# Kernel optimization log

Hardware: AMD Instinct MI355X
Metric: run time of the kernel (lower is better)

## Reference

```python
import jax, jax.numpy as jnp
import numpy as np

N_NUM = 8
N_CAT = 4
CARD = 100
D_NUM = 16
D_CAT = 16
D_OUT = N_NUM * D_NUM + N_CAT * D_CAT  # 192
D_HID = 256
TEMP = 1.0


def setup_inputs() -> dict:
    key = jax.random.key(0)
    ks = jax.random.split(key, 12)
    B, N = 512, 131072
    x_num = jax.random.normal(ks[0], (B, N_NUM), dtype=jnp.float32)
    x_cat = jax.random.randint(ks[1], (B, N_CAT), 0, CARD)
    cand_x_num = jax.random.normal(ks[2], (N, N_NUM), dtype=jnp.float32)
    cand_x_cat = jax.random.randint(ks[3], (N, N_CAT), 0, CARD)
    cand_y = jax.random.uniform(ks[4], (N, 10), dtype=jnp.float32)
    s = 0.05
    W_num = jax.random.normal(ks[5], (N_NUM, D_NUM), dtype=jnp.float32) * s
    b_num = jax.random.normal(ks[6], (N_NUM, D_NUM), dtype=jnp.float32) * s
    emb = jax.random.normal(ks[7], (N_CAT, CARD, D_CAT), dtype=jnp.float32) * s
    W1 = jax.random.normal(ks[8], (D_OUT, D_HID), dtype=jnp.float32) * s
    b1 = jnp.zeros((D_HID,), dtype=jnp.float32)
    W2 = jax.random.normal(ks[9], (D_HID, D_OUT), dtype=jnp.float32) * s
    b2 = jnp.zeros((D_OUT,), dtype=jnp.float32)
    return dict(x_num=x_num, x_cat=x_cat, cand_x_num=cand_x_num,
                cand_x_cat=cand_x_cat, cand_y=cand_y, W_num=W_num, b_num=b_num,
                emb=emb, W1=W1, b1=b1, W2=W2, b2=b2)


def _encode(x_num, x_cat, W_num, b_num, emb):
    # per-numerical-feature linear embedding: [B, n_num, d_num]
    num_e = x_num[:, :, None] * W_num[None] + b_num[None]
    # categorical lookup: emb[f, x_cat[:, f]] -> [B, n_cat, d_cat]
    cat_e = emb[jnp.arange(N_CAT)[None, :], x_cat]
    B = x_num.shape[0]
    return jnp.concatenate([num_e.reshape(B, -1), cat_e.reshape(B, -1)], axis=-1)


def _block(z, W1, b1, W2, b2):
    # residual MLP block: d_out -> hidden -> d_out
    return z + jax.nn.relu(z @ W1 + b1) @ W2 + b2


def reference(x_num, x_cat, cand_x_num, cand_x_cat, cand_y,
              W_num, b_num, emb, W1, b1, W2, b2):
    x = _encode(x_num, x_cat, W_num, b_num, emb)            # [B, d]
    c = _encode(cand_x_num, cand_x_cat, W_num, b_num, emb)  # [N, d]
    x = _block(x, W1, b1, W2, b2)
    c = _block(c, W1, b1, W2, b2)
    d2 = (jnp.sum(x * x, axis=-1)[:, None] + jnp.sum(c * c, axis=-1)[None, :]
          - 2.0 * (x @ c.T))
    dist = jnp.sqrt(jnp.maximum(d2, 0.0)) / TEMP            # [B, N]
    probs = jax.nn.softmax(-dist, axis=-1)
    return probs @ cand_y                                    # [B, 10]
```

## Files before the change

### kernel.cpp

```cpp
#include <hip/hip_runtime.h>
#include <hip/hip_bf16.h>

typedef __bf16 bf16;
typedef __attribute__((ext_vector_type(8))) __bf16 bf16x8;
typedef __attribute__((ext_vector_type(4))) __bf16 bf16x4;
typedef __attribute__((ext_vector_type(4))) float f32x4;

#define NQ     512
#define NC     131072
#define DIM    192
#define HID    256
#define NY     10
#define NSLICE 512

#define KL2E   2.0813689810056077f
#define N2KL2E -4.1627379620112154f

#define OFF_W1B 0u
#define OFF_W2B (OFF_W1B + 98304u)
#define OFF_XE8 (OFF_W2B + 98304u)
#define OFF_X2  (OFF_XE8 + 98304u)
#define OFF_CE8 (OFF_X2 + 2048u)
#define OFF_C2  (OFF_CE8 + 25165824u)
#define OFF_P   (OFF_C2 + 524288u)
#define OFF_YB  (OFF_P + 12582912u)

__global__ __launch_bounds__(256) void k_prep(const float* __restrict__ W1,
                                              const float* __restrict__ W2,
                                              const float* __restrict__ cy,
                                              bf16* __restrict__ W1B,
                                              bf16* __restrict__ W2B,
                                              bf16* __restrict__ YB) {
  if (blockIdx.x < 384) {
    int idx = blockIdx.x * 256 + threadIdx.x;
    if (idx < 192 * 256) {
      int k = idx / 256, n = idx % 256;
      int p = (k >> 5) * 4 + ((k >> 3) & 3);
      W1B[((size_t)(p * 256 + n)) * 8 + (k & 7)] = (bf16)W1[idx];
    } else {
      int i2 = idx - 192 * 256;
      int k = i2 / 192, n = i2 % 192;
      int p = (k >> 5) * 4 + ((k >> 3) & 3);
      W2B[((size_t)(p * 192 + n)) * 8 + (k & 7)] = (bf16)W2[i2];
    }
  } else {
    int u = (blockIdx.x - 384) * 256 + threadIdx.x;
    int p32 = u >> 6, lane6 = u & 63;
    int qq = lane6 >> 4, l15 = lane6 & 15;
    bf16x8 v;
#pragma unroll
    for (int jj = 0; jj < 8; jj++) {
      int cand = p32 * 32 + qq * 8 + jj;
      float x = (l15 < 10) ? cy[(size_t)cand * NY + l15] : (l15 == 10 ? 1.f : 0.f);
      v[jj] = (bf16)x;
    }
    *(bf16x8*)&YB[(size_t)u * 8] = v;
  }
}

__global__ __launch_bounds__(256, 3) void k_encode(
    const float* __restrict__ xnq, const int* __restrict__ xcq,
    const float* __restrict__ xnc, const int* __restrict__ xcc,
    const float* __restrict__ Wn, const float* __restrict__ bn,
    const float* __restrict__ emb, const float* __restrict__ b1,
    const float* __restrict__ b2, const bf16* __restrict__ W1B,
    const bf16* __restrict__ W2B, unsigned char* __restrict__ ce8,
    unsigned char* __restrict__ xe8, float* __restrict__ x2v,
    float* __restrict__ c2v) {
  __shared__ alignas(16) bf16 zt[64][200];
  __shared__ alignas(16) bf16 hth[64][136];
  __shared__ float n2l[64];
  unsigned char* zs = (unsigned char*)&hth[0][0];

  const int t = threadIdx.x;
  const bool isq = blockIdx.x < 8;
  const int row0 = (isq ? blockIdx.x : blockIdx.x - 8) * 64;
  const float* __restrict__ xn = isq ? xnq : xnc;
  const int* __restrict__ xc = isq ? xcq : xcc;
  const int lane = t & 63, w = t >> 6;
  const int l15 = lane & 15, q = lane >> 4;

  if (t < 64) n2l[t] = 0.f;

  {
    const int g = row0 + lane;
    float2 xv2 = *(const float2*)&xn[(size_t)g * 8 + 2 * w];
    int cv = xc[g * 4 + w];
#pragma unroll
    for (int f01 = 0; f01 < 2; f01++) {
      int f = 2 * w + f01;
      float xv = f01 ? xv2.y : xv2.x;
      f32x4 wv[4], bv[4];
#pragma unroll
      for (int i = 0; i < 4; i++) {
        wv[i] = *(const f32x4*)&Wn[f * 16 + i * 4];
        bv[i] = *(const f32x4*)&bn[f * 16 + i * 4];
      }
      bf16x8 p0, p1;
#pragma unroll
      for (int u = 0; u < 8; u++) {
        p0[u] = (bf16)(xv * wv[u >> 2][u & 3] + bv[u >> 2][u & 3]);
        p1[u] = (bf16)(xv * wv[2 + (u >> 2)][u & 3] + bv[2 + (u >> 2)][u & 3]);
      }
      *(bf16x8*)&zt[lane][f * 16] = p0;
      *(bf16x8*)&zt[lane][f * 16 + 8] = p1;
    }
    const float* er = &emb[(size_t)(w * 100 + cv) * 16];
    f32x4 e0 = *(const f32x4*)&er[0];
    f32x4 e1 = *(const f32x4*)&er[4];
    f32x4 e2 = *(const f32x4*)&er[8];
    f32x4 e3 = *(const f32x4*)&er[12];
    bf16x8 pc0, pc1;
#pragma unroll
    for (int u = 0; u < 4; u++) {
      pc0[u] = (bf16)e0[u]; pc0[4 + u] = (bf16)e1[u];
      pc1[u] = (bf16)e2[u]; pc1[4 + u] = (bf16)e3[u];
    }
    *(bf16x8*)&zt[lane][128 + w * 16] = pc0;
    *(bf16x8*)&zt[lane][128 + w * 16 + 8] = pc1;
  }
  __syncthreads();

  f32x4 z4 = {0.f, 0.f, 0.f, 0.f};
  f32x4 acc2[4][3];
#pragma unroll
  for (int mi = 0; mi < 4; mi++)
#pragma unroll
    for (int ni = 0; ni < 3; ni++) acc2[mi][ni] = z4;

#pragma unroll
  for (int h = 0; h < 2; ++h) {
    if (h) __syncthreads();

    {
      f32x4 acc1[4][2];
#pragma unroll
      for (int mi = 0; mi < 4; mi++)
#pragma unroll
        for (int ni = 0; ni < 2; ni++) acc1[mi][ni] = z4;
#pragma unroll 2
      for (int kk = 0; kk < 192; kk += 32) {
        bf16x8 a[4], b[2];
#pragma unroll
        for (int mi = 0; mi < 4; mi++)
          a[mi] = *(const bf16x8*)&zt[mi * 16 + l15][kk + q * 8];
        const bf16* wp = &W1B[(size_t)(((kk >> 5) * 4 + q) * 256 + h * 128 + w * 32 + l15) * 8];
#pragma unroll
        for (int ni = 0; ni < 2; ni++)
          b[ni] = *(const bf16x8*)&wp[ni * 128];
#pragma unroll
        for (int mi = 0; mi < 4; mi++)
#pragma unroll
          for (int ni = 0; ni < 2; ni++)
            acc1[mi][ni] = __builtin_amdgcn_mfma_f32_16x16x32_bf16(a[mi], b[ni], acc1[mi][ni], 0, 0, 0);
      }
#pragma unroll
      for (int ni = 0; ni < 2; ni++) {
        int nl = w * 32 + ni * 16 + l15;
        float bb = b1[h * 128 + nl];
#pragma unroll
        for (int mi = 0; mi < 4; mi++)
#pragma unroll
          for (int r = 0; r < 4; r++) {
            float hv = acc1[mi][ni][r] + bb;
            hth[mi * 16 + q * 4 + r][nl] = (bf16)(hv > 0.f ? hv : 0.f);
          }
      }
    }
    __syncthreads();

#pragma unroll 2
    for (int kk2 = 0; kk2 < 128; kk2 += 32) {
      bf16x8 a[4], b[3];
#pragma unroll
      for (int mi = 0; mi < 4; mi++)
        a[mi] = *(const bf16x8*)&hth[mi * 16 + l15][kk2 + q * 8];
      const bf16* wp = &W2B[(size_t)(((h * 4 + (kk2 >> 5)) * 4 + q) * 192 + w * 48 + l15) * 8];
#pragma unroll
      for (int ni = 0; ni < 3; ni++)
        b[ni] = *(const bf16x8*)&wp[ni * 128];
#pragma unroll
      for (int mi = 0; mi < 4; mi++)
#pragma unroll
        for (int ni = 0; ni < 3; ni++)
          acc2[mi][ni] = __builtin_amdgcn_mfma_f32_16x16x32_bf16(a[mi], b[ni], acc2[mi][ni], 0, 0, 0);
    }
  }
  __syncthreads();

  {
    float nrm[4][4];
#pragma unroll
    for (int mi = 0; mi < 4; mi++)
#pragma unroll
      for (int r = 0; r < 4; r++) nrm[mi][r] = 0.f;
#pragma unroll
    for (int ni = 0; ni < 3; ni++) {
      int n = w * 48 + ni * 16 + l15;
      float bb = b2[n];
#pragma unroll
      for (int mi = 0; mi < 4; mi++)
#pragma unroll
        for (int r = 0; r < 4; r++) {
          int rr = mi * 16 + q * 4 + r;
          float v = (float)zt[rr][n] + acc2[mi][ni][r] + bb;
          int pk = __builtin_amdgcn_cvt_pk_fp8_f32(v, v, 0, false);
          zs[rr * 208 + n] = (unsigned char)(pk & 0xff);
          float vr = __builtin_amdgcn_cvt_f32_fp8(pk, 0);
          nrm[mi][r] += vr * vr;
        }
    }
#pragma unroll
    for (int mi = 0; mi < 4; mi++)
#pragma unroll
      for (int r = 0; r < 4; r++) {
        float s = nrm[mi][r];
        s += __shfl_xor(s, 1);
        s += __shfl_xor(s, 2);
        s += __shfl_xor(s, 4);
        s += __shfl_xor(s, 8);
        if (l15 == 0) atomicAdd(&n2l[mi * 16 + q * 4 + r], s);
      }
  }
  __syncthreads();

  if (isq) {
    for (int cc = w; cc < 24; cc += 4) {
      long v = *(const long*)&zs[lane * 208 + cc * 8];
      *(long*)&xe8[((size_t)cc * NQ + row0 + lane) * 8] = v;
    }
    if (t < 64) x2v[row0 + t] = n2l[t] * KL2E;
  } else {
    unsigned int* dst = (unsigned int*)(ce8 + (size_t)row0 * DIM);
#pragma unroll
    for (int i = 0; i < 12; i++) {
      int j = t + 256 * i;
      int r = j / 48, cb = (j - r * 48) * 4;
      dst[j] = *(const unsigned int*)&zs[r * 208 + cb];
    }
    if (t < 64) c2v[row0 + t] = n2l[t] * KL2E;
  }
}

__global__ __launch_bounds__(256, 3) void k_dist(
    const unsigned char* __restrict__ xe8, const float* __restrict__ x2v,
    const unsigned char* __restrict__ ce8, const float* __restrict__ c2v,
    const bf16* __restrict__ YB, float* __restrict__ P) {
  __shared__ alignas(16) unsigned char ct8[64][208];
  __shared__ alignas(16) bf16 ET[4][16][72];

  const int t = threadIdx.x;
  const int slice = blockIdx.x & (NSLICE - 1);
  const int half = blockIdx.x >> 9;
  const int n0 = slice * 256;
  const int qh = half * 256;
  const int lane = t & 63, w = t >> 6;
  const int l15 = lane & 15, q = lane >> 4;
  const int qbase = qh + w * 64;

  f32x4 z4 = {0.f, 0.f, 0.f, 0.f};
  f32x4 oacc[4];
#pragma unroll
  for (int nq = 0; nq < 4; nq++) oacc[nq] = z4;

  float x2a[4];
#pragma unroll
  for (int nq = 0; nq < 4; nq++) x2a[nq] = x2v[qbase + nq * 16 + l15];

#pragma unroll 1
  for (int c = 0; c < 4; ++c) {
    if (c) __syncthreads();
    {
      int sr = t >> 2, squ = t & 3;
      const uint4* src = (const uint4*)(ce8 + (size_t)(n0 + c * 64 + sr) * DIM + squ * 48);
      uint4* dst = (uint4*)&ct8[sr][squ * 48];
#pragma unroll
      for (int i = 0; i < 3; i++) dst[i] = src[i];
    }
    __syncthreads();

    bf16x8 yf[2];
#pragma unroll
    for (int kb = 0; kb < 2; kb++)
      yf[kb] = *(const bf16x8*)&YB[((size_t)((slice * 8) + c * 2 + kb) * 64 + lane) * 8];
    f32x4 c2r[4];
#pragma unroll
    for (int mc = 0; mc < 4; mc++)
      c2r[mc] = *(const f32x4*)&c2v[n0 + c * 64 + mc * 16 + q * 4];

    f32x4 acc[4][4];
#pragma unroll
    for (int mc = 0; mc < 4; mc++)
#pragma unroll
      for (int nq = 0; nq < 4; nq++) acc[mc][nq] = z4;

#pragma unroll 1
    for (int kk = 0; kk < 192; kk += 32) {
      long a[4], b[4];
#pragma unroll
      for (int mc = 0; mc < 4; mc++)
        a[mc] = *(const long*)&ct8[mc * 16 + l15][kk + q * 8];
      const unsigned char* xp = &xe8[(size_t)(((kk >> 5) * 4 + q) * NQ + qbase + l15) * 8];
#pragma unroll
      for (int nq = 0; nq < 4; nq++)
        b[nq] = *(const long*)&xp[nq * 128];
#pragma unroll
      for (int mc = 0; mc < 4; mc++)
#pragma unroll
        for (int nq = 0; nq < 4; nq++)
          acc[mc][nq] = __builtin_amdgcn_mfma_f32_16x16x32_fp8_fp8(a[mc], b[nq], acc[mc][nq], 0, 0, 0);
    }

#pragma unroll
    for (int nq = 0; nq < 4; ++nq) {
#pragma unroll
      for (int mc = 0; mc < 4; mc++) {
        bf16x4 ev;
#pragma unroll
        for (int r = 0; r < 4; r++) {
          float d2 = __builtin_fmaf(N2KL2E, acc[mc][nq][r], x2a[nq] + c2r[mc][r]);
          ev[r] = (bf16)__builtin_amdgcn_exp2f(-__builtin_amdgcn_sqrtf(__builtin_fabsf(d2)));
        }
        *(bf16x4*)&ET[w][l15][mc * 16 + q * 4] = ev;
      }
#pragma unroll
      for (int kb = 0; kb < 2; kb++) {
        bf16x8 a = *(const bf16x8*)&ET[w][l15][kb * 32 + q * 8];
        oacc[nq] = __builtin_amdgcn_mfma_f32_16x16x32_bf16(a, yf[kb], oacc[nq], 0, 0, 0);
      }
    }
  }

  __syncthreads();
  float* Pst = (float*)&ct8[0][0];
  if (l15 < 11) {
#pragma unroll
    for (int nq = 0; nq < 4; nq++)
#pragma unroll
      for (int r = 0; r < 4; r++) {
        int lq = w * 64 + nq * 16 + q * 4 + r;
        Pst[lq * 12 + l15] = oacc[nq][r];
      }
  }
  __syncthreads();
  {
    f32x4* Pg = (f32x4*)(P + (size_t)blockIdx.x * 3072);
    const f32x4* Ps = (const f32x4*)Pst;
#pragma unroll
    for (int i = t; i < 768; i += 256) Pg[i] = Ps[i];
  }
}

__global__ __launch_bounds__(512) void k_comb(const float* __restrict__ P,
                                              float* __restrict__ out) {
  __shared__ float red[8][11];
  const int t = threadIdx.x;
  const int qy = blockIdx.x;
  const int lane = t & 63, w = t >> 6;

  const float* p = &P[((size_t)((qy >> 8) * 512 + t) * 256 + (qy & 255)) * 12];
  f32x4 v0 = *(const f32x4*)&p[0];
  f32x4 v1 = *(const f32x4*)&p[4];
  f32x4 v2 = *(const f32x4*)&p[8];
  float s[11];
#pragma unroll
  for (int j = 0; j < 4; j++) s[j] = v0[j];
#pragma unroll
  for (int j = 0; j < 4; j++) s[4 + j] = v1[j];
#pragma unroll
  for (int j = 0; j < 3; j++) s[8 + j] = v2[j];
#pragma unroll
  for (int d = 1; d < 64; d <<= 1)
#pragma unroll
    for (int j = 0; j < 11; j++) s[j] += __shfl_xor(s[j], d);
  if (lane == 0)
#pragma unroll
    for (int j = 0; j < 11; j++) red[w][j] = s[j];
  __syncthreads();
  if (t < 10) {
    float o = 0.f, l = 0.f;
#pragma unroll
    for (int i = 0; i < 8; i++) { o += red[i][t]; l += red[i][10]; }
    out[qy * NY + t] = o / l;
  }
}

extern "C" void kernel_launch(void* const* d_in, const int* in_sizes, int n_in,
                              void* d_out, int out_size, void* d_ws, size_t ws_size,
                              hipStream_t stream) {
  (void)in_sizes; (void)n_in; (void)out_size; (void)ws_size;
  const float* x_num = (const float*)d_in[0];
  const int*   x_cat = (const int*)d_in[1];
  const float* c_num = (const float*)d_in[2];
  const int*   c_cat = (const int*)d_in[3];
  const float* c_y   = (const float*)d_in[4];
  const float* W_num = (const float*)d_in[5];
  const float* b_num = (const float*)d_in[6];
  const float* emb   = (const float*)d_in[7];
  const float* W1    = (const float*)d_in[8];
  const float* b1    = (const float*)d_in[9];
  const float* W2    = (const float*)d_in[10];
  const float* b2    = (const float*)d_in[11];
  float* out = (float*)d_out;

  char* ws = (char*)d_ws;
  bf16*  W1B = (bf16*)(ws + OFF_W1B);
  bf16*  W2B = (bf16*)(ws + OFF_W2B);
  unsigned char* xe8 = (unsigned char*)(ws + OFF_XE8);
  float* x2v = (float*)(ws + OFF_X2);
  unsigned char* ce8 = (unsigned char*)(ws + OFF_CE8);
  float* c2v = (float*)(ws + OFF_C2);
  float* P   = (float*)(ws + OFF_P);
  bf16*  YB  = (bf16*)(ws + OFF_YB);

  k_prep<<<dim3(1408), dim3(256), 0, stream>>>(W1, W2, c_y, W1B, W2B, YB);
  k_encode<<<dim3(8 + NC / 64), dim3(256), 0, stream>>>(
      x_num, x_cat, c_num, c_cat, W_num, b_num, emb, b1, b2, W1B, W2B,
      ce8, xe8, x2v, c2v);
  k_dist<<<dim3(2 * NSLICE), dim3(256), 0, stream>>>(xe8, x2v, ce8, c2v, YB, P);
  k_comb<<<dim3(NQ), dim3(512), 0, stream>>>(P, out);
}
```

Measured before the change: 177.9 us.

## Run encoder MLP in FP8 MFMA with single-pass hidden layer

Switches the encoder's two MLP matmuls from bf16 to fp8 MFMA. It stores weights, inputs and hidden activations as fp8 in workspace and shared memory. The hidden layer is now computed in one 256-wide pass instead of two 128-wide halves, which removes a barrier-separated loop. Smaller shared-memory tiles allow raising the occupancy hint to four blocks per CU. The cost is lower precision in the hidden activations and weights, which may move outputs further from the reference.

Measured after the change: 166.4 us. 6.4% less time.

```diff
diff --git a/kernel.cpp b/kernel.cpp
--- a/kernel.cpp
+++ b/kernel.cpp
@@ -17,31 +17,39 @@
 #define N2KL2E -4.1627379620112154f
 
 #define OFF_W1B 0u
-#define OFF_W2B (OFF_W1B + 98304u)
-#define OFF_XE8 (OFF_W2B + 98304u)
+#define OFF_W2B (OFF_W1B + 49152u)
+#define OFF_XE8 (OFF_W2B + 49152u)
 #define OFF_X2  (OFF_XE8 + 98304u)
 #define OFF_CE8 (OFF_X2 + 2048u)
 #define OFF_C2  (OFF_CE8 + 25165824u)
 #define OFF_P   (OFF_C2 + 524288u)
 #define OFF_YB  (OFF_P + 12582912u)
 
+static __device__ __forceinline__ unsigned pk4(float a, float b, float c, float d) {
+  unsigned w = __builtin_amdgcn_cvt_pk_fp8_f32(a, b, 0, false);
+  w = __builtin_amdgcn_cvt_pk_fp8_f32(c, d, w, true);
+  return w;
+}
+
 __global__ __launch_bounds__(256) void k_prep(const float* __restrict__ W1,
                                               const float* __restrict__ W2,
                                               const float* __restrict__ cy,
-                                              bf16* __restrict__ W1B,
-                                              bf16* __restrict__ W2B,
+                                              unsigned char* __restrict__ W1B8,
+                                              unsigned char* __restrict__ W2B8,
                                               bf16* __restrict__ YB) {
   if (blockIdx.x < 384) {
     int idx = blockIdx.x * 256 + threadIdx.x;
     if (idx < 192 * 256) {
       int k = idx / 256, n = idx % 256;
       int p = (k >> 5) * 4 + ((k >> 3) & 3);
-      W1B[((size_t)(p * 256 + n)) * 8 + (k & 7)] = (bf16)W1[idx];
+      int pk = __builtin_amdgcn_cvt_pk_fp8_f32(W1[idx], W1[idx], 0, false);
+      W1B8[((size_t)(p * 256 + n)) * 8 + (k & 7)] = (unsigned char)(pk & 0xff);
     } else {
       int i2 = idx - 192 * 256;
       int k = i2 / 192, n = i2 % 192;
       int p = (k >> 5) * 4 + ((k >> 3) & 3);
-      W2B[((size_t)(p * 192 + n)) * 8 + (k & 7)] = (bf16)W2[i2];
+      int pk = __builtin_amdgcn_cvt_pk_fp8_f32(W2[i2], W2[i2], 0, false);
+      W2B8[((size_t)(p * 192 + n)) * 8 + (k & 7)] = (unsigned char)(pk & 0xff);
     }
   } else {
     int u = (blockIdx.x - 384) * 256 + threadIdx.x;
@@ -58,19 +66,18 @@
   }
 }
 
-__global__ __launch_bounds__(256, 3) void k_encode(
+__global__ __launch_bounds__(256, 4) void k_encode(
     const float* __restrict__ xnq, const int* __restrict__ xcq,
     const float* __restrict__ xnc, const int* __restrict__ xcc,
     const float* __restrict__ Wn, const float* __restrict__ bn,
     const float* __restrict__ emb, const float* __restrict__ b1,
-    const float* __restrict__ b2, const bf16* __restrict__ W1B,
-    const bf16* __restrict__ W2B, unsigned char* __restrict__ ce8,
+    const float* __restrict__ b2, const unsigned char* __restrict__ W1B8,
+    const unsigned char* __restrict__ W2B8, unsigned char* __restrict__ ce8,
     unsigned char* __restrict__ xe8, float* __restrict__ x2v,
     float* __restrict__ c2v) {
-  __shared__ alignas(16) bf16 zt[64][200];
-  __shared__ alignas(16) bf16 hth[64][136];
+  __shared__ alignas(16) unsigned char zt8[64][208];
+  __shared__ alignas(16) unsigned char hth8[64][264];
   __shared__ float n2l[64];
-  unsigned char* zs = (unsigned char*)&hth[0][0];
 
   const int t = threadIdx.x;
   const bool isq = blockIdx.x < 8;
@@ -90,103 +97,97 @@
     for (int f01 = 0; f01 < 2; f01++) {
       int f = 2 * w + f01;
       float xv = f01 ? xv2.y : xv2.x;
-      f32x4 wv[4], bv[4];
+      float zz[16];
 #pragma unroll
       for (int i = 0; i < 4; i++) {
-        wv[i] = *(const f32x4*)&Wn[f * 16 + i * 4];
-        bv[i] = *(const f32x4*)&bn[f * 16 + i * 4];
+        f32x4 wv = *(const f32x4*)&Wn[f * 16 + i * 4];
+        f32x4 bv = *(const f32x4*)&bn[f * 16 + i * 4];
+#pragma unroll
+        for (int u = 0; u < 4; u++) zz[i * 4 + u] = xv * wv[u] + bv[u];
       }
-      bf16x8 p0, p1;
-#pragma unroll
-      for (int u = 0; u < 8; u++) {
-        p0[u] = (bf16)(xv * wv[u >> 2][u & 3] + bv[u >> 2][u & 3]);
-        p1[u] = (bf16)(xv * wv[2 + (u >> 2)][u & 3] + bv[2 + (u >> 2)][u & 3]);
-      }
-      *(bf16x8*)&zt[lane][f * 16] = p0;
-      *(bf16x8*)&zt[lane][f * 16 + 8] = p1;
+      uint4 pk;
+      pk.x = pk4(zz[0], zz[1], zz[2], zz[3]);
+      pk.y = pk4(zz[4], zz[5], zz[6], zz[7]);
+      pk.z = pk4(zz[8], zz[9], zz[10], zz[11]);
+      pk.w = pk4(zz[12], zz[13], zz[14], zz[15]);
+      *(uint4*)&zt8[lane][f * 16] = pk;
     }
     const float* er = &emb[(size_t)(w * 100 + cv) * 16];
     f32x4 e0 = *(const f32x4*)&er[0];
     f32x4 e1 = *(const f32x4*)&er[4];
     f32x4 e2 = *(const f32x4*)&er[8];
     f32x4 e3 = *(const f32x4*)&er[12];
-    bf16x8 pc0, pc1;
-#pragma unroll
-    for (int u = 0; u < 4; u++) {
-      pc0[u] = (bf16)e0[u]; pc0[4 + u] = (bf16)e1[u];
-      pc1[u] = (bf16)e2[u]; pc1[4 + u] = (bf16)e3[u];
-    }
-    *(bf16x8*)&zt[lane][128 + w * 16] = pc0;
-    *(bf16x8*)&zt[lane][128 + w * 16 + 8] = pc1;
+    uint4 pk;
+    pk.x = pk4(e0[0], e0[1], e0[2], e0[3]);
+    pk.y = pk4(e1[0], e1[1], e1[2], e1[3]);
+    pk.z = pk4(e2[0], e2[1], e2[2], e2[3]);
+    pk.w = pk4(e3[0], e3[1], e3[2], e3[3]);
+    *(uint4*)&zt8[lane][128 + w * 16] = pk;
   }
   __syncthreads();
 
   f32x4 z4 = {0.f, 0.f, 0.f, 0.f};
+
+  {
+    f32x4 acc1[4][4];
+#pragma unroll
+    for (int mi = 0; mi < 4; mi++)
+#pragma unroll
+      for (int ni = 0; ni < 4; ni++) acc1[mi][ni] = z4;
+#pragma unroll 2
+    for (int kk = 0; kk < 192; kk += 32) {
+      long a[4], b[4];
+#pragma unroll
+      for (int mi = 0; mi < 4; mi++)
+        a[mi] = *(const long*)&zt8[mi * 16 + l15][kk + q * 8];
+      const unsigned char* wp = &W1B8[(size_t)(((kk >> 5) * 4 + q) * 256 + w * 64 + l15) * 8];
+#pragma unroll
+      for (int ni = 0; ni < 4; ni++)
+        b[ni] = *(const long*)&wp[ni * 128];
+#pragma unroll
+      for (int mi = 0; mi < 4; mi++)
+#pragma unroll
+        for (int ni = 0; ni < 4; ni++)
+          acc1[mi][ni] = __builtin_amdgcn_mfma_f32_16x16x32_fp8_fp8(a[mi], b[ni], acc1[mi][ni], 0, 0, 0);
+    }
+#pragma unroll
+    for (int ni = 0; ni < 4; ni++) {
+      int n = w * 64 + ni * 16 + l15;
+      float bb = b1[n];
+#pragma unroll
+      for (int mi = 0; mi < 4; mi++)
+#pragma unroll
+        for (int r = 0; r < 4; r++) {
+          float hv = acc1[mi][ni][r] + bb;
+          hv = hv > 0.f ? hv : 0.f;
+          int pk = __builtin_amdgcn_cvt_pk_fp8_f32(hv, hv, 0, false);
+          hth8[mi * 16 + q * 4 + r][n] = (unsigned char)(pk & 0xff);
+        }
+    }
+  }
+  __syncthreads();
+
   f32x4 acc2[4][3];
 #pragma unroll
   for (int mi = 0; mi < 4; mi++)
 #pragma unroll
     for (int ni = 0; ni < 3; ni++) acc2[mi][ni] = z4;
-
-#pragma unroll
-  for (int h = 0; h < 2; ++h) {
-    if (h) __syncthreads();
-
-    {
-      f32x4 acc1[4][2];
-#pragma unroll
-      for (int mi = 0; mi < 4; mi++)
-#pragma unroll
-        for (int ni = 0; ni < 2; ni++) acc1[mi][ni] = z4;
 #pragma unroll 2
-      for (int kk = 0; kk < 192; kk += 32) {
-        bf16x8 a[4], b[2];
-#pragma unroll
-        for (int mi = 0; mi < 4; mi++)
-          a[mi] = *(const bf16x8*)&zt[mi * 16 + l15][kk + q * 8];
-        const bf16* wp = &W1B[(size_t)(((kk >> 5) * 4 + q) * 256 + h * 128 + w * 32 + l15) * 8];
-#pragma unroll
-        for (int ni = 0; ni < 2; ni++)
-          b[ni] = *(const bf16x8*)&wp[ni * 128];
-#pragma unroll
-        for (int mi = 0; mi < 4; mi++)
-#pragma unroll
-          for (int ni = 0; ni < 2; ni++)
-            acc1[mi][ni] = __builtin_amdgcn_mfma_f32_16x16x32_bf16(a[mi], b[ni], acc1[mi][ni], 0, 0, 0);
-      }
-#pragma unroll
-      for (int ni = 0; ni < 2; ni++) {
-        int nl = w * 32 + ni * 16 + l15;
-        float bb = b1[h * 128 + nl];
-#pragma unroll
-        for (int mi = 0; mi < 4; mi++)
-#pragma unroll
-          for (int r = 0; r < 4; r++) {
-            float hv = acc1[mi][ni][r] + bb;
-            hth[mi * 16 + q * 4 + r][nl] = (bf16)(hv > 0.f ? hv : 0.f);
-          }
-      }
-    }
-    __syncthreads();
-
-#pragma unroll 2
-    for (int kk2 = 0; kk2 < 128; kk2 += 32) {
-      bf16x8 a[4], b[3];
-#pragma unroll
-      for (int mi = 0; mi < 4; mi++)
-        a[mi] = *(const bf16x8*)&hth[mi * 16 + l15][kk2 + q * 8];
-      const bf16* wp = &W2B[(size_t)(((h * 4 + (kk2 >> 5)) * 4 + q) * 192 + w * 48 + l15) * 8];
+  for (int kk = 0; kk < 256; kk += 32) {
+    long a[4], b[3];
+#pragma unroll
+    for (int mi = 0; mi < 4; mi++)
+      a[mi] = *(const long*)&hth8[mi * 16 + l15][kk + q * 8];
+    const unsigned char* wp = &W2B8[(size_t)(((kk >> 5) * 4 + q) * 192 + w * 48 + l15) * 8];
+#pragma unroll
+    for (int ni = 0; ni < 3; ni++)
+      b[ni] = *(const long*)&wp[ni * 128];
+#pragma unroll
+    for (int mi = 0; mi < 4; mi++)
 #pragma unroll
       for (int ni = 0; ni < 3; ni++)
-        b[ni] = *(const bf16x8*)&wp[ni * 128];
-#pragma unroll
-      for (int mi = 0; mi < 4; mi++)
-#pragma unroll
-        for (int ni = 0; ni < 3; ni++)
-          acc2[mi][ni] = __builtin_amdgcn_mfma_f32_16x16x32_bf16(a[mi], b[ni], acc2[mi][ni], 0, 0, 0);
-    }
-  }
-  __syncthreads();
+        acc2[mi][ni] = __builtin_amdgcn_mfma_f32_16x16x32_fp8_fp8(a[mi], b[ni], acc2[mi][ni], 0, 0, 0);
+  }
 
   {
     float nrm[4][4];
@@ -203,9 +204,10 @@
 #pragma unroll
         for (int r = 0; r < 4; r++) {
           int rr = mi * 16 + q * 4 + r;
-          float v = (float)zt[rr][n] + acc2[mi][ni][r] + bb;
+          float zf = __builtin_amdgcn_cvt_f32_fp8((int)zt8[rr][n], 0);
+          float v = zf + acc2[mi][ni][r] + bb;
           int pk = __builtin_amdgcn_cvt_pk_fp8_f32(v, v, 0, false);
-          zs[rr * 208 + n] = (unsigned char)(pk & 0xff);
+          zt8[rr][n] = (unsigned char)(pk & 0xff);
           float vr = __builtin_amdgcn_cvt_f32_fp8(pk, 0);
           nrm[mi][r] += vr * vr;
         }
@@ -226,7 +228,7 @@
 
   if (isq) {
     for (int cc = w; cc < 24; cc += 4) {
-      long v = *(const long*)&zs[lane * 208 + cc * 8];
+      long v = *(const long*)&zt8[lane][cc * 8];
       *(long*)&xe8[((size_t)cc * NQ + row0 + lane) * 8] = v;
     }
     if (t < 64) x2v[row0 + t] = n2l[t] * KL2E;
@@ -236,7 +238,7 @@
     for (int i = 0; i < 12; i++) {
       int j = t + 256 * i;
       int r = j / 48, cb = (j - r * 48) * 4;
-      dst[j] = *(const unsigned int*)&zs[r * 208 + cb];
+      dst[j] = *(const unsigned int*)&zt8[r][cb];
     }
     if (t < 64) c2v[row0 + t] = n2l[t] * KL2E;
   }
@@ -404,18 +406,18 @@
   float* out = (float*)d_out;
 
   char* ws = (char*)d_ws;
-  bf16*  W1B = (bf16*)(ws + OFF_W1B);
-  bf16*  W2B = (bf16*)(ws + OFF_W2B);
-  unsigned char* xe8 = (unsigned char*)(ws + OFF_XE8);
+  unsigned char* W1B8 = (unsigned char*)(ws + OFF_W1B);
+  unsigned char* W2B8 = (unsigned char*)(ws + OFF_W2B);
+  unsigned char* xe8  = (unsigned char*)(ws + OFF_XE8);
   float* x2v = (float*)(ws + OFF_X2);
-  unsigned char* ce8 = (unsigned char*)(ws + OFF_CE8);
+  unsigned char* ce8  = (unsigned char*)(ws + OFF_CE8);
   float* c2v = (float*)(ws + OFF_C2);
   float* P   = (float*)(ws + OFF_P);
   bf16*  YB  = (bf16*)(ws + OFF_YB);
 
-  k_prep<<<dim3(1408), dim3(256), 0, stream>>>(W1, W2, c_y, W1B, W2B, YB);
+  k_prep<<<dim3(1408), dim3(256), 0, stream>>>(W1, W2, c_y, W1B8, W2B8, YB);
   k_encode<<<dim3(8 + NC / 64), dim3(256), 0, stream>>>(
-      x_num, x_cat, c_num, c_cat, W_num, b_num, emb, b1, b2, W1B, W2B,
+      x_num, x_cat, c_num, c_cat, W_num, b_num, emb, b1, b2, W1B8, W2B8,
       ce8, xe8, x2v, c2v);
   k_dist<<<dim3(2 * NSLICE), dim3(256), 0, stream>>>(xe8, x2v, ce8, c2v, YB, P);
   k_comb<<<dim3(NQ), dim3(512), 0, stream>>>(P, out);
```
